# Kernel tuning notes

Hardware: AMD Instinct MI355X
Metric: run time of the kernel (lower is better)

## Reference

```python
import jax, jax.numpy as jnp
import numpy as np

BOX_WARP = 1.2
BMIN, BMAX = -0.6, 0.6   # sampler bbox
EPS_FD = 0.01            # finite-difference eps for SDF normals
RADIUS = 0.5             # sphere sdf bias radius
INV_S = 80.0             # sdf -> density sharpness (softplus clamp mode)
S_PER_RAY = 96


def _grid_sample_one(feat, uv):
    # feat: [C,H,W]; uv: [M,2] in [-1,1]; bilinear, align_corners=False, zeros padding
    C, H, W = feat.shape
    x = ((uv[:, 0] + 1.0) * W - 1.0) * 0.5
    y = ((uv[:, 1] + 1.0) * H - 1.0) * 0.5
    x0 = jnp.floor(x).astype(jnp.int32)
    y0 = jnp.floor(y).astype(jnp.int32)
    wx = x - x0
    wy = y - y0

    def g(ix, iy):
        valid = ((ix >= 0) & (ix < W) & (iy >= 0) & (iy < H)).astype(feat.dtype)
        v = feat[:, jnp.clip(iy, 0, H - 1), jnp.clip(ix, 0, W - 1)]  # [C,M]
        return v * valid[None, :]

    out = (g(x0, y0) * (1 - wx) * (1 - wy) + g(x0 + 1, y0) * wx * (1 - wy)
           + g(x0, y0 + 1) * (1 - wx) * wy + g(x0 + 1, y0 + 1) * wx * wy)
    return out.T  # [M,C]


def sample_from_planes(planes, coords):
    # planes: [N,3,C,H,W]; coords: [N,M,3] -> [N,M,3*C]
    N, P, C, H, W = planes.shape
    M = coords.shape[1]
    nc = coords * (2.0 / BOX_WARP)
    proj = jnp.stack([nc[..., (0, 1)], nc[..., (0, 2)], nc[..., (1, 2)]], axis=1)  # [N,3,M,2]
    s = jax.vmap(_grid_sample_one)(planes.reshape(N * P, C, H, W), proj.reshape(N * P, M, 2))
    return s.reshape(N, P, M, C).transpose(0, 2, 1, 3).reshape(N, M, P * C)


def decode(planes, coords, W1, b1, W2, b2):
    x = sample_from_planes(planes, coords)
    return jax.nn.relu(x @ W1 + b1) @ W2 + b2  # [N,M,4]


def render(planes, ro, rd, W1, b1, W2, b2):
    N, R, _ = ro.shape
    S = S_PER_RAY
    safe_rd = jnp.where(jnp.abs(rd) < 1e-9, 1e-9, rd)
    t1 = (BMIN - ro) / safe_rd
    t2 = (BMAX - ro) / safe_rd
    tn = jnp.maximum(jnp.max(jnp.minimum(t1, t2), axis=-1), 0.0)   # [N,R] ray_start (auto box)
    tf = jnp.min(jnp.maximum(t1, t2), axis=-1)                      # [N,R] ray_end
    span = jnp.maximum(tf - tn, 0.0)
    frac = (jnp.arange(S, dtype=ro.dtype) + 0.5) / S
    depths = tn[..., None] + span[..., None] * frac                 # [N,R,S]
    pts = (ro[:, :, None, :] + depths[..., None] * rd[:, :, None, :]).reshape(N, R * S, 3)

    x = decode(planes, pts, W1, b1, W2, b2)
    sdf = x[..., 0:1]
    rgb = jax.nn.sigmoid(x[..., 1:]) * (1 + 2 * 0.001) - 0.001

    # finite-difference SDF gradient (3 extra decoder passes)
    eye = jnp.eye(3, dtype=pts.dtype) * EPS_FD
    sdf_off = jnp.stack(
        [decode(planes, jnp.clip(pts + eye[i], BMIN, BMAX), W1, b1, W2, b2)[..., 0] for i in range(3)],
        axis=-1)                                                    # [N,M,3]
    sdf_grad = (sdf_off - sdf) / EPS_FD
    normal = sdf_grad / (jnp.linalg.norm(sdf_grad, axis=-1, keepdims=True) + 1e-8)

    # sphere sdf bias, sdf -> density, alpha compositing
    shifted = sdf[..., 0] + (jnp.linalg.norm(pts, axis=-1) - RADIUS)
    sigma = jax.nn.softplus(-shifted * INV_S).reshape(N, R, S)
    delta = (span / S)[..., None]
    alpha = 1.0 - jnp.exp(-sigma * delta)
    T = jnp.cumprod(1.0 - alpha + 1e-10, axis=-1)
    T = jnp.concatenate([jnp.ones_like(T[..., :1]), T[..., :-1]], axis=-1)
    w = alpha * T                                                   # [N,R,S]

    rgb_s = (w[..., None] * rgb.reshape(N, R, S, 3)).sum(-2)
    wsum = w.sum(-1, keepdims=True)
    rgb_s = rgb_s + (1.0 - wsum)                                    # white background
    depth_s = (w * depths).sum(-1, keepdims=True)
    normal_s = (w[..., None] * normal.reshape(N, R, S, 3)).sum(-2)
    return rgb_s, depth_s, wsum, sdf_grad, normal_s


def reference(planes, ray_origins, ray_directions, W1, b1, W2, b2, render_size):
    N = planes.shape[0]
    rgb_s, depth_s, wsum, sdf_grad, normal_s = render(planes, ray_origins, ray_directions, W1, b1, W2, b2)
    n = normal_s / (jnp.linalg.norm(normal_s, axis=-1, keepdims=True) + 1e-8)
    n = (n + 1.0) * 0.5
    n = n * wsum  # lerp(0, n, opacity)
    H = W = render_size
    comp_rgb = rgb_s.transpose(0, 2, 1).reshape(N, 3, H, W)
    comp_depth = depth_s.transpose(0, 2, 1).reshape(N, 1, H, W)
    opacity = wsum.transpose(0, 2, 1).reshape(N, 1, H, W)
    comp_normal = n.transpose(0, 2, 1).reshape(N, 3, H, W)
    return (comp_rgb, comp_depth, opacity, comp_normal, sdf_grad)


def setup_inputs():
    key = jax.random.key(0)
    k0, k1, k2 = jax.random.split(key, 3)
    N, C, Hp, rs = 1, 80, 64, 64
    planes = jax.random.normal(k0, (N, 3, C, Hp, Hp), jnp.float32)
    u = jnp.linspace(-0.45, 0.45, rs)
    uu, vv = jnp.meshgrid(u, u, indexing='xy')
    d = jnp.stack([uu, vv, -jnp.ones_like(uu)], -1).reshape(-1, 3)
    d = d / jnp.linalg.norm(d, axis=-1, keepdims=True)
    ray_directions = jnp.broadcast_to(d, (N, rs * rs, 3)).astype(jnp.float32)
    ray_origins = jnp.broadcast_to(jnp.array([0.0, 0.0, 1.5], jnp.float32), (N, rs * rs, 3))
    W1 = jax.random.normal(k1, (3 * C, 64), jnp.float32) * 0.05
    b1 = jnp.zeros((64,), jnp.float32)
    W2 = jax.random.normal(k2, (64, 4), jnp.float32) * 0.05
    b2 = jnp.zeros((4,), jnp.float32)
    return {"planes": planes, "ray_origins": ray_origins, "ray_directions": ray_directions,
            "W1": W1, "b1": b1, "W2": W2, "b2": b2, "render_size": rs}
```

## Files before the change

kernel.cpp:

```cpp
#include <hip/hip_runtime.h>
#include <hip/hip_bf16.h>

#define NUM_RAYS 4096
#define S_PER 96
#define NPTS (NUM_RAYS * S_PER)
#define CCH 80
#define HID 64

#define WSB_W2     256
#define WSB_B1     1536
#define WSB_B2     1856
#define WSB_W1S    4096
#define WSB_PT     40960



typedef __attribute__((ext_vector_type(8))) short short8;
typedef __attribute__((ext_vector_type(4))) float f32x4;
typedef __attribute__((ext_vector_type(2))) float f32x2;

__device__ __forceinline__ float bf2f(__hip_bfloat16 v) { return __bfloat162float(v); }

__device__ __forceinline__ short f2bs(float f) {
  __hip_bfloat16 h = __float2bfloat16(f);
  short s; __builtin_memcpy(&s, &h, 2); return s;
}

template <bool BF16>
__device__ __forceinline__ float ldin(const void* p, size_t i) {
  if (BF16) return bf2f(((const __hip_bfloat16*)p)[i]);
  else      return ((const float*)p)[i];
}
template <bool BF16>
__device__ __forceinline__ void stout(void* p, size_t i, float v) {
  if (BF16) ((__hip_bfloat16*)p)[i] = __float2bfloat16(v);
  else      ((float*)p)[i] = v;
}

__device__ __forceinline__ f32x2 unpk2(unsigned u) {
  f32x2 r;
  r.x = __uint_as_float(u << 16);
  r.y = __uint_as_float(u);
  return r;
}

__device__ __forceinline__ unsigned pack_bf16(float lo, float hi) {
#if __has_builtin(__builtin_amdgcn_cvt_pk_bf16_f32)
  typedef __attribute__((ext_vector_type(2))) __bf16 b2t;
  b2t r = __builtin_amdgcn_cvt_pk_bf16_f32(lo, hi);
  unsigned u; __builtin_memcpy(&u, &r, 4); return u;
#else
  unsigned ul = __float_as_uint(lo) + 0x8000u;
  unsigned uh = __float_as_uint(hi) + 0x8000u;
  return __builtin_amdgcn_perm(uh, ul, 0x07060302);
#endif
}

__device__ __forceinline__ bool detect_bf16(const void* rdv) {
  int lane = threadIdx.x & 63;
  const __hip_bfloat16* p = (const __hip_bfloat16*)rdv;
  float x = bf2f(p[lane * 3 + 0]);
  float y = bf2f(p[lane * 3 + 1]);
  float z = bf2f(p[lane * 3 + 2]);
  float n2 = x * x + y * y + z * z;
  bool ok = (n2 > 0.95f) && (n2 < 1.05f);
  return __ballot(ok) == ~0ull;
}

template <bool BF16>
__device__ __forceinline__ void prep_body(const void* __restrict__ W1,
                                          const void* __restrict__ b1,
                                          const void* __restrict__ W2,
                                          const void* __restrict__ b2,
                                          float* __restrict__ ws, int tid) {
  unsigned short* w1sw = (unsigned short*)((char*)ws + WSB_W1S);
  if (tid < 15360) {
    int p = tid / 5120;
    int r = tid - p * 5120;
    int ch, n;
    if (r < 4096) {
      int ccl  = r >> 11;
      int r2   = r & 2047;
      int j    = r2 & 7;
      int lane = (r2 >> 3) & 63;
      int nb   = r2 >> 9;
      ch = ccl * 32 + 8 * (lane >> 4) + j;
      n  = nb * 16 + (lane & 15);
    } else {
      int r2   = r - 4096;
      int j    = r2 & 7;
      int l31  = (r2 >> 3) & 31;
      int nb   = r2 >> 8;
      ch = 64 + 8 * (l31 >> 4) + j;
      n  = nb * 16 + (l31 & 15);
    }
    w1sw[tid] = (unsigned short)f2bs(ldin<BF16>(W1, (size_t)(p * 80 + ch) * 64 + n));
  }
  float* w2f = (float*)((char*)ws + WSB_W2);
  float* b1f = (float*)((char*)ws + WSB_B1);
  float* b2f = (float*)((char*)ws + WSB_B2);
  if (tid < 256) w2f[tid] = ldin<BF16>(W2, tid);
  if (tid < 64)  b1f[tid] = ldin<BF16>(b1, tid);
  if (tid < 4)   b2f[tid] = ldin<BF16>(b2, tid);
}

template <bool BF16>
__device__ __forceinline__ void transpose_body(const void* __restrict__ planes,
                                               float* __restrict__ ws) {
  int b  = blockIdx.x;
  int tt = b & 15;
  int ct = (b >> 4) % 5;
  int p  = b / 80;
  int tex = tt * 256 + threadIdx.x;
  unsigned u[8];
  #pragma unroll
  for (int i = 0; i < 8; i++) {
    int c0 = ct * 16 + 2 * i;
    float v0 = ldin<BF16>(planes, ((size_t)(p * 80 + c0) * 4096) + tex);
    float v1 = ldin<BF16>(planes, ((size_t)(p * 80 + c0 + 1) * 4096) + tex);
    unsigned s0 = (unsigned short)f2bs(v0);
    unsigned s1 = (unsigned short)f2bs(v1);
    u[i] = s0 | (s1 << 16);
  }
  unsigned short* ptb = (unsigned short*)((char*)ws + WSB_PT);
  uint4* dst = (uint4*)(ptb + ((size_t)(p * 4096 + tex) * 80 + ct * 16));
  dst[0] = make_uint4(u[0], u[1], u[2], u[3]);
  dst[1] = make_uint4(u[4], u[5], u[6], u[7]);
}

__global__ void setup_kernel(const void* __restrict__ planes,
                             const void* __restrict__ W1,
                             const void* __restrict__ b1,
                             const void* __restrict__ W2,
                             const void* __restrict__ b2,
                             const void* __restrict__ rd,
                             float* __restrict__ ws) {
  bool bf = detect_bf16(rd);
  if (blockIdx.x < 240) {
    if (bf) transpose_body<true >(planes, ws);
    else    transpose_body<false>(planes, ws);
  } else {
    int tid = (blockIdx.x - 240) * 256 + threadIdx.x;
    if (bf) prep_body<true >(W1, b1, W2, b2, ws, tid);
    else    prep_body<false>(W1, b1, W2, b2, ws, tid);
  }
}

struct TapInfo {
  float w00, w10, w01, w11;
  int o00, o10, o01, o11;
};
__device__ __forceinline__ TapInfo tap_setup(float u, float v) {
  TapInfo t;
  float fx = u * 32.0f + 31.5f;
  float fy = v * 32.0f + 31.5f;
  float flx = floorf(fx), fly = floorf(fy);
  int x0 = (int)flx, y0 = (int)fly;
  float wx = fx - flx, wy = fy - fly;
  int x1 = x0 + 1, y1 = y0 + 1;
  bool vx0 = (x0 >= 0) && (x0 < 64);
  bool vx1 = (x1 >= 0) && (x1 < 64);
  bool vy0 = (y0 >= 0) && (y0 < 64);
  bool vy1 = (y1 >= 0) && (y1 < 64);
  int cx0 = min(max(x0, 0), 63), cx1 = min(max(x1, 0), 63);
  int cy0 = min(max(y0, 0), 63), cy1 = min(max(y1, 0), 63);
  t.w00 = (1.0f - wx) * (1.0f - wy) * ((vx0 && vy0) ? 1.0f : 0.0f);
  t.w10 = wx * (1.0f - wy)          * ((vx1 && vy0) ? 1.0f : 0.0f);
  t.w01 = (1.0f - wx) * wy          * ((vx0 && vy1) ? 1.0f : 0.0f);
  t.w11 = wx * wy                   * ((vx1 && vy1) ? 1.0f : 0.0f);
  t.o00 = cy0 * 64 + cx0; t.o10 = cy0 * 64 + cx1;
  t.o01 = cy1 * 64 + cx0; t.o11 = cy1 * 64 + cx1;
  return t;
}

template <bool BF16>
__device__ __forceinline__ void fused_body(const void* __restrict__ ro,
                                           const void* __restrict__ rd,
                                           const float* __restrict__ ws,
                                           void* __restrict__ out,
                                           unsigned short* __restrict__ w1s,
                                           float (*__restrict__ rec)[7],
                                           float* __restrict__ w2s,
                                           float* __restrict__ xfer,
                                           float (*__restrict__ red)[8]) {
  const unsigned short* ptb = (const unsigned short*)((const char*)ws + WSB_PT);
  const float* w2f = (const float*)((const char*)ws + WSB_W2);
  const float* b1f = (const float*)((const char*)ws + WSB_B1);
  const float* b2f = (const float*)((const char*)ws + WSB_B2);

  int tid = threadIdx.x;
  int wave = tid >> 6;
  int lane = tid & 63;
  int lane15 = lane & 15;
  int quad = lane >> 4;
  int ray = blockIdx.x;

  {
    const uint4* src = (const uint4*)((const char*)ws + WSB_W1S);
    uint4* dst = (uint4*)w1s;
    #pragma unroll
    for (int t = 0; t < 8; t++) {
      int idx = tid + 256 * t;
      if (idx < 1920) dst[idx] = src[idx];
    }
  }
  if (tid < 256) w2s[tid] = w2f[tid];

  float ox = ldin<BF16>(ro, (size_t)ray*3+0), oy = ldin<BF16>(ro, (size_t)ray*3+1), oz = ldin<BF16>(ro, (size_t)ray*3+2);
  float dx = ldin<BF16>(rd, (size_t)ray*3+0), dy = ldin<BF16>(rd, (size_t)ray*3+1), dz = ldin<BF16>(rd, (size_t)ray*3+2);
  float o3[3] = {ox, oy, oz}, d3[3] = {dx, dy, dz};
  float tmin = -1e30f, tmax = 1e30f;
  #pragma unroll
  for (int k = 0; k < 3; k++) {
    float sd = (fabsf(d3[k]) < 1e-9f) ? 1e-9f : d3[k];
    float ta = (-0.6f - o3[k]) / sd;
    float tb = ( 0.6f - o3[k]) / sd;
    tmin = fmaxf(tmin, fminf(ta, tb));
    tmax = fminf(tmax, fmaxf(ta, tb));
  }
  float tn = fmaxf(tmin, 0.0f);
  float span = fmaxf(tmax - tn, 0.0f);
  float delta = span * (1.0f / (float)S_PER);
  float b1x[4];
  #pragma unroll
  for (int nb = 0; nb < 4; nb++) b1x[nb] = b1f[nb * 16 + lane15];

  __syncthreads();

  #pragma unroll 1
  for (int it = 0; it < 6; it++) {
    int sbase = it * 16 + wave * 4;

    int sF = sbase + (lane15 >> 2);
    int d  = lane15 & 3;
    float depF = tn + span * (((float)sF + 0.5f) * (1.0f / (float)S_PER));
    float px = ox + depF * dx, py = oy + depF * dy, pz = oz + depF * dz;
    if (d == 1) px += 0.01f;
    if (d == 2) py += 0.01f;
    if (d == 3) pz += 0.01f;
    if (d > 0) {
      px = fminf(fmaxf(px, -0.6f), 0.6f);
      py = fminf(fmaxf(py, -0.6f), 0.6f);
      pz = fminf(fmaxf(pz, -0.6f), 0.6f);
    }
    const float inv = 1.0f / 0.6f;
    float ux = px * inv, uy = py * inv, uz = pz * inv;

    f32x4 acc[4];
    #pragma unroll
    for (int nb = 0; nb < 4; nb++) acc[nb] = (f32x4){0.f, 0.f, 0.f, 0.f};

    #pragma unroll 1
    for (int p = 0; p < 3; p++) {
      float u = (p == 2) ? uy : ux;
      float v = (p == 0) ? uy : uz;
      TapInfo t = tap_setup(u, v);
      const unsigned short* c00p = ptb + (size_t)p * 327680 + t.o00 * 80 + 8 * quad;
      const unsigned short* c10p = ptb + (size_t)p * 327680 + t.o10 * 80 + 8 * quad;
      const unsigned short* c01p = ptb + (size_t)p * 327680 + t.o01 * 80 + 8 * quad;
      const unsigned short* c11p = ptb + (size_t)p * 327680 + t.o11 * 80 + 8 * quad;
      f32x2 wv00 = {t.w00, t.w00}, wv10 = {t.w10, t.w10};
      f32x2 wv01 = {t.w01, t.w01}, wv11 = {t.w11, t.w11};
      const unsigned short* w1p = w1s + p * 5120;
      #pragma unroll
      for (int ccl = 0; ccl < 3; ccl++) {
        int4 afi = {0, 0, 0, 0};
        if (ccl < 2 || quad < 2) {
          uint4 q00 = *(const uint4*)(c00p + 32 * ccl);
          uint4 q10 = *(const uint4*)(c10p + 32 * ccl);
          uint4 q01 = *(const uint4*)(c01p + 32 * ccl);
          uint4 q11 = *(const uint4*)(c11p + 32 * ccl);
          unsigned u00[4] = {q00.x, q00.y, q00.z, q00.w};
          unsigned u10[4] = {q10.x, q10.y, q10.z, q10.w};
          unsigned u01[4] = {q01.x, q01.y, q01.z, q01.w};
          unsigned u11[4] = {q11.x, q11.y, q11.z, q11.w};
          int ae[4];
          #pragma unroll
          for (int q = 0; q < 4; q++) {
            f32x2 f = unpk2(u00[q]) * wv00;
            f = __builtin_elementwise_fma(unpk2(u10[q]), wv10, f);
            f = __builtin_elementwise_fma(unpk2(u01[q]), wv01, f);
            f = __builtin_elementwise_fma(unpk2(u11[q]), wv11, f);
            ae[q] = (int)pack_bf16(f.x, f.y);
          }
          afi.x = ae[0]; afi.y = ae[1]; afi.z = ae[2]; afi.w = ae[3];
        }
        short8 afr;
        __builtin_memcpy(&afr, &afi, 16);
        #pragma unroll
        for (int nb = 0; nb < 4; nb++) {
          int boff = (ccl < 2) ? (ccl * 2048 + (nb * 64 + lane) * 8)
                               : (4096 + (nb * 32 + (lane & 31)) * 8);
          short8 bfr = *(const short8*)(w1p + boff);
          acc[nb] = __builtin_amdgcn_mfma_f32_16x16x32_bf16(afr, bfr, acc[nb], 0, 0, 0);
        }
      }
    }

    float vals[7];
    #pragma unroll
    for (int k = 0; k < 7; k++) vals[k] = 0.0f;
    #pragma unroll
    for (int nb = 0; nb < 4; nb++) {
      float4 w2r = *(const float4*)(w2s + (nb * 16 + lane15) * 4);
      float hr0 = fmaxf(acc[nb][0] + b1x[nb], 0.0f);
      vals[0] = fmaf(hr0, w2r.x, vals[0]);
      vals[4] = fmaf(hr0, w2r.y, vals[4]);
      vals[5] = fmaf(hr0, w2r.z, vals[5]);
      vals[6] = fmaf(hr0, w2r.w, vals[6]);
      float hr1 = fmaxf(acc[nb][1] + b1x[nb], 0.0f);
      float hr2 = fmaxf(acc[nb][2] + b1x[nb], 0.0f);
      float hr3 = fmaxf(acc[nb][3] + b1x[nb], 0.0f);
      vals[1] = fmaf(hr1, w2r.x, vals[1]);
      vals[2] = fmaf(hr2, w2r.x, vals[2]);
      vals[3] = fmaf(hr3, w2r.x, vals[3]);
    }
    #pragma unroll
    for (int mask = 1; mask < 16; mask <<= 1) {
      #pragma unroll
      for (int k = 0; k < 7; k++) vals[k] += __shfl_xor(vals[k], mask, 64);
    }

    if (lane15 == 0) {
      int sE = sbase + quad;
      #pragma unroll
      for (int k = 0; k < 7; k++) rec[sE][k] = vals[k];
    }
  }

  __syncthreads();

  float b2_0 = b2f[0], b2_1 = b2f[1], b2_2 = b2f[2], b2_3 = b2f[3];
  float a = 0.f, l = 0.f, pcr = 0.f, pcg = 0.f, pcb = 0.f, pnx = 0.f, pny = 0.f, pnz = 0.f, pdt = 0.f;
  if (tid < S_PER) {
    float v0 = rec[tid][0], v1 = rec[tid][1], v2 = rec[tid][2], v3 = rec[tid][3];
    float v4 = rec[tid][4], v5 = rec[tid][5], v6 = rec[tid][6];
    float sdf0 = v0 + b2_0;
    float g0 = (v1 - v0) * 100.0f;
    float g1 = (v2 - v0) * 100.0f;
    float g2 = (v3 - v0) * 100.0f;
    size_t gid = (size_t)ray * S_PER + tid;
    stout<BF16>(out, (size_t)32768 + gid * 3 + 0, g0);
    stout<BF16>(out, (size_t)32768 + gid * 3 + 1, g1);
    stout<BF16>(out, (size_t)32768 + gid * 3 + 2, g2);
    pcr = 1.0f / (1.0f + expf(-(v4 + b2_1))) * 1.002f - 0.001f;
    pcg = 1.0f / (1.0f + expf(-(v5 + b2_2))) * 1.002f - 0.001f;
    pcb = 1.0f / (1.0f + expf(-(v6 + b2_3))) * 1.002f - 0.001f;
    pdt = tn + span * (((float)tid + 0.5f) * (1.0f / (float)S_PER));
    float ex = ox + pdt * dx, ey = oy + pdt * dy, ez = oz + pdt * dz;
    float pn = sqrtf(ex * ex + ey * ey + ez * ez);
    float shifted = sdf0 + pn - 0.5f;
    float xarg = -shifted * 80.0f;
    float sigma = (xarg > 20.0f) ? xarg : log1pf(expf(xarg));
    a = 1.0f - expf(-sigma * delta);
    float gl = sqrtf(g0 * g0 + g1 * g1 + g2 * g2) + 1e-8f;
    float igl = 1.0f / gl;
    pnx = g0 * igl; pny = g1 * igl; pnz = g2 * igl;
    l = logf(1.0f - a + 1e-10f);
  }

  float lv = l;
  #pragma unroll
  for (int off = 1; off < 64; off <<= 1) {
    float up = __shfl_up(lv, off, 64);
    if (lane >= off) lv += up;
  }
  if (tid == 63) xfer[0] = lv;
  __syncthreads();
  if (tid >= 64 && tid < S_PER) lv += xfer[0];

  float T = expf(lv - l);
  float w = (tid < S_PER) ? a * T : 0.0f;
  float q[8];
  q[0] = w;
  q[1] = w * pcr; q[2] = w * pcg; q[3] = w * pcb;
  q[4] = w * pnx; q[5] = w * pny; q[6] = w * pnz;
  q[7] = w * pdt;
  #pragma unroll
  for (int off = 1; off < 64; off <<= 1) {
    #pragma unroll
    for (int k = 0; k < 8; k++) q[k] += __shfl_xor(q[k], off, 64);
  }
  if (lane == 0) {
    #pragma unroll
    for (int k = 0; k < 8; k++) red[wave][k] = q[k];
  }
  __syncthreads();
  if (tid == 0) {
    float R[8];
    #pragma unroll
    for (int k = 0; k < 8; k++) R[k] = red[0][k] + red[1][k] + red[2][k] + red[3][k];
    float wsum = R[0];
    float nl = sqrtf(R[4] * R[4] + R[5] * R[5] + R[6] * R[6]) + 1e-8f;
    float inl = 1.0f / nl;
    float nrm3[3] = {R[4], R[5], R[6]};
    float rgb3[3] = {R[1], R[2], R[3]};
    #pragma unroll
    for (int c = 0; c < 3; c++) {
      float n = (nrm3[c] * inl + 1.0f) * 0.5f * wsum;
      stout<BF16>(out, (size_t)(c * 4096 + ray), rgb3[c] + 1.0f - wsum);
      stout<BF16>(out, (size_t)(20480 + c * 4096 + ray), n);
    }
    stout<BF16>(out, (size_t)(12288 + ray), R[7]);
    stout<BF16>(out, (size_t)(16384 + ray), wsum);
  }
}

__global__ __launch_bounds__(256) void fused_kernel(
    const void* __restrict__ ro,
    const void* __restrict__ rd,
    const float* __restrict__ ws,
    void* __restrict__ out) {
  __shared__ __align__(16) unsigned short w1s[15360];
  __shared__ float rec[S_PER][7];
  __shared__ float w2s[256];
  __shared__ float xfer[1];
  __shared__ float red[4][8];

  if (detect_bf16(rd)) fused_body<true >(ro, rd, ws, out, w1s, rec, w2s, xfer, red);
  else                 fused_body<false>(ro, rd, ws, out, w1s, rec, w2s, xfer, red);
}

extern "C" void kernel_launch(void* const* d_in, const int* in_sizes, int n_in,
                              void* d_out, int out_size, void* d_ws, size_t ws_size,
                              hipStream_t stream) {
  const void* planes = d_in[0];
  const void* ro     = d_in[1];
  const void* rd     = d_in[2];
  const void* W1     = d_in[3];
  const void* b1     = d_in[4];
  const void* W2     = d_in[5];
  const void* b2     = d_in[6];
  float* ws = (float*)d_ws;

  setup_kernel<<<304, 256, 0, stream>>>(planes, W1, b1, W2, b2, rd, ws);
  fused_kernel<<<NUM_RAYS, 256, 0, stream>>>(ro, rd, ws, d_out);
}
```

Measured before the change: 266.7 us.

## Software-pipeline triplane gathers across planes with double-buffered register loads

Computes the tap setup for all three planes up front and unrolls the plane/channel-chunk loop. Loads for the next chunk are issued before blending and running MFMA on the current one, so gather latency is hidden behind math. Also moves the offset multiply into tap_setup, drops a redundant guard on the w2 copy, and sets launch bounds to ask for 4 waves per SIMD. The cost is higher register pressure, which may cause spills under the new occupancy bound.

```diff
diff --git a/kernel.cpp b/kernel.cpp
--- a/kernel.cpp
+++ b/kernel.cpp
@@ -168,8 +168,8 @@
   t.w10 = wx * (1.0f - wy)          * ((vx1 && vy0) ? 1.0f : 0.0f);
   t.w01 = (1.0f - wx) * wy          * ((vx0 && vy1) ? 1.0f : 0.0f);
   t.w11 = wx * wy                   * ((vx1 && vy1) ? 1.0f : 0.0f);
-  t.o00 = cy0 * 64 + cx0; t.o10 = cy0 * 64 + cx1;
-  t.o01 = cy1 * 64 + cx0; t.o11 = cy1 * 64 + cx1;
+  t.o00 = cy0 * 5120 + cx0 * 80; t.o10 = cy0 * 5120 + cx1 * 80;
+  t.o01 = cy1 * 5120 + cx0 * 80; t.o11 = cy1 * 5120 + cx1 * 80;
   return t;
 }
 
@@ -204,7 +204,7 @@
       if (idx < 1920) dst[idx] = src[idx];
     }
   }
-  if (tid < 256) w2s[tid] = w2f[tid];
+  w2s[tid] = w2f[tid];
 
   float ox = ldin<BF16>(ro, (size_t)ray*3+0), oy = ldin<BF16>(ro, (size_t)ray*3+1), oz = ldin<BF16>(ro, (size_t)ray*3+2);
   float dx = ldin<BF16>(rd, (size_t)ray*3+0), dy = ldin<BF16>(rd, (size_t)ray*3+1), dz = ldin<BF16>(rd, (size_t)ray*3+2);
@@ -227,6 +227,8 @@
 
   __syncthreads();
 
+  const unsigned short* pbase = ptb + 8 * quad;
+
   #pragma unroll 1
   for (int it = 0; it < 6; it++) {
     int sbase = it * 16 + wave * 4;
@@ -246,56 +248,71 @@
     const float inv = 1.0f / 0.6f;
     float ux = px * inv, uy = py * inv, uz = pz * inv;
 
+    TapInfo tp0 = tap_setup(ux, uy);
+    TapInfo tp1 = tap_setup(ux, uz);
+    TapInfo tp2 = tap_setup(uy, uz);
+
     f32x4 acc[4];
     #pragma unroll
     for (int nb = 0; nb < 4; nb++) acc[nb] = (f32x4){0.f, 0.f, 0.f, 0.f};
 
-    #pragma unroll 1
-    for (int p = 0; p < 3; p++) {
-      float u = (p == 2) ? uy : ux;
-      float v = (p == 0) ? uy : uz;
-      TapInfo t = tap_setup(u, v);
-      const unsigned short* c00p = ptb + (size_t)p * 327680 + t.o00 * 80 + 8 * quad;
-      const unsigned short* c10p = ptb + (size_t)p * 327680 + t.o10 * 80 + 8 * quad;
-      const unsigned short* c01p = ptb + (size_t)p * 327680 + t.o01 * 80 + 8 * quad;
-      const unsigned short* c11p = ptb + (size_t)p * 327680 + t.o11 * 80 + 8 * quad;
-      f32x2 wv00 = {t.w00, t.w00}, wv10 = {t.w10, t.w10};
-      f32x2 wv01 = {t.w01, t.w01}, wv11 = {t.w11, t.w11};
-      const unsigned short* w1p = w1s + p * 5120;
-      #pragma unroll
-      for (int ccl = 0; ccl < 3; ccl++) {
-        int4 afi = {0, 0, 0, 0};
-        if (ccl < 2 || quad < 2) {
-          uint4 q00 = *(const uint4*)(c00p + 32 * ccl);
-          uint4 q10 = *(const uint4*)(c10p + 32 * ccl);
-          uint4 q01 = *(const uint4*)(c01p + 32 * ccl);
-          uint4 q11 = *(const uint4*)(c11p + 32 * ccl);
-          unsigned u00[4] = {q00.x, q00.y, q00.z, q00.w};
-          unsigned u10[4] = {q10.x, q10.y, q10.z, q10.w};
-          unsigned u01[4] = {q01.x, q01.y, q01.z, q01.w};
-          unsigned u11[4] = {q11.x, q11.y, q11.z, q11.w};
-          int ae[4];
-          #pragma unroll
-          for (int q = 0; q < 4; q++) {
-            f32x2 f = unpk2(u00[q]) * wv00;
-            f = __builtin_elementwise_fma(unpk2(u10[q]), wv10, f);
-            f = __builtin_elementwise_fma(unpk2(u01[q]), wv01, f);
-            f = __builtin_elementwise_fma(unpk2(u11[q]), wv11, f);
-            ae[q] = (int)pack_bf16(f.x, f.y);
-          }
-          afi.x = ae[0]; afi.y = ae[1]; afi.z = ae[2]; afi.w = ae[3];
-        }
-        short8 afr;
-        __builtin_memcpy(&afr, &afi, 16);
-        #pragma unroll
-        for (int nb = 0; nb < 4; nb++) {
-          int boff = (ccl < 2) ? (ccl * 2048 + (nb * 64 + lane) * 8)
-                               : (4096 + (nb * 32 + (lane & 31)) * 8);
-          short8 bfr = *(const short8*)(w1p + boff);
-          acc[nb] = __builtin_amdgcn_mfma_f32_16x16x32_bf16(afr, bfr, acc[nb], 0, 0, 0);
-        }
-      }
-    }
+    uint4 A0, A1, A2, A3, B0, B1, B2, B3;
+
+#define LOAD4(D0, D1, D2, D3, TP, P, CCL)                                     \
+    do {                                                                      \
+      if ((CCL) < 2 || quad < 2) {                                            \
+        const unsigned short* bp_ = pbase + (size_t)(P) * 327680 + 32 * (CCL);\
+        D0 = *(const uint4*)(bp_ + TP.o00);                                   \
+        D1 = *(const uint4*)(bp_ + TP.o10);                                   \
+        D2 = *(const uint4*)(bp_ + TP.o01);                                   \
+        D3 = *(const uint4*)(bp_ + TP.o11);                                   \
+      }                                                                       \
+    } while (0)
+
+#define BLEND(S0, S1, S2, S3, TP, P, CCL)                                     \
+    do {                                                                      \
+      int4 afi = {0, 0, 0, 0};                                                \
+      if ((CCL) < 2 || quad < 2) {                                            \
+        f32x2 wv00 = {TP.w00, TP.w00}, wv10 = {TP.w10, TP.w10};               \
+        f32x2 wv01 = {TP.w01, TP.w01}, wv11 = {TP.w11, TP.w11};               \
+        unsigned u00[4] = {S0.x, S0.y, S0.z, S0.w};                           \
+        unsigned u10[4] = {S1.x, S1.y, S1.z, S1.w};                           \
+        unsigned u01[4] = {S2.x, S2.y, S2.z, S2.w};                           \
+        unsigned u11[4] = {S3.x, S3.y, S3.z, S3.w};                           \
+        int ae[4];                                                            \
+        _Pragma("unroll")                                                     \
+        for (int q = 0; q < 4; q++) {                                         \
+          f32x2 f = unpk2(u00[q]) * wv00;                                     \
+          f = __builtin_elementwise_fma(unpk2(u10[q]), wv10, f);              \
+          f = __builtin_elementwise_fma(unpk2(u01[q]), wv01, f);              \
+          f = __builtin_elementwise_fma(unpk2(u11[q]), wv11, f);              \
+          ae[q] = (int)pack_bf16(f.x, f.y);                                   \
+        }                                                                     \
+        afi.x = ae[0]; afi.y = ae[1]; afi.z = ae[2]; afi.w = ae[3];           \
+      }                                                                       \
+      short8 afr;                                                             \
+      __builtin_memcpy(&afr, &afi, 16);                                       \
+      _Pragma("unroll")                                                       \
+      for (int nb = 0; nb < 4; nb++) {                                        \
+        int boff = ((CCL) < 2) ? ((CCL) * 2048 + (nb * 64 + lane) * 8)        \
+                               : (4096 + (nb * 32 + (lane & 31)) * 8);        \
+        short8 bfr = *(const short8*)(w1s + (P) * 5120 + boff);               \
+        acc[nb] = __builtin_amdgcn_mfma_f32_16x16x32_bf16(afr, bfr, acc[nb], 0, 0, 0); \
+      }                                                                       \
+    } while (0)
+
+    LOAD4(A0, A1, A2, A3, tp0, 0, 0);
+    LOAD4(B0, B1, B2, B3, tp0, 0, 1);  BLEND(A0, A1, A2, A3, tp0, 0, 0);
+    LOAD4(A0, A1, A2, A3, tp0, 0, 2);  BLEND(B0, B1, B2, B3, tp0, 0, 1);
+    LOAD4(B0, B1, B2, B3, tp1, 1, 0);  BLEND(A0, A1, A2, A3, tp0, 0, 2);
+    LOAD4(A0, A1, A2, A3, tp1, 1, 1);  BLEND(B0, B1, B2, B3, tp1, 1, 0);
+    LOAD4(B0, B1, B2, B3, tp1, 1, 2);  BLEND(A0, A1, A2, A3, tp1, 1, 1);
+    LOAD4(A0, A1, A2, A3, tp2, 2, 0);  BLEND(B0, B1, B2, B3, tp1, 1, 2);
+    LOAD4(B0, B1, B2, B3, tp2, 2, 1);  BLEND(A0, A1, A2, A3, tp2, 2, 0);
+    LOAD4(A0, A1, A2, A3, tp2, 2, 2);  BLEND(B0, B1, B2, B3, tp2, 2, 1);
+                                       BLEND(A0, A1, A2, A3, tp2, 2, 2);
+#undef LOAD4
+#undef BLEND
 
     float vals[7];
     #pragma unroll
@@ -406,7 +423,7 @@
   }
 }
 
-__global__ __launch_bounds__(256) void fused_kernel(
+__global__ __launch_bounds__(256, 4) void fused_kernel(
     const void* __restrict__ ro,
     const void* __restrict__ rd,
     const float* __restrict__ ws,
```

Result: slower. 771.1 us (+189.1%).
